# Performance work log

Hardware: AMD Instinct MI355X
Metric: run time of the kernel (lower is better)

Reference implementation:

```python
import jax, jax.numpy as jnp
import numpy as np

N = 50000      # nodes
E = 800000     # edges (avg degree 16)
IN = 64        # in_channels
H = 128        # hidden_channels
OUT = 64       # out_channels
G = 64         # number of graphs in batch


def setup_inputs() -> dict:
    key = jax.random.key(0)
    ks = jax.random.split(key, 16)
    x = jax.random.normal(ks[0], (N, IN), dtype=jnp.float32)
    edge_index = jax.random.randint(ks[1], (2, E), 0, N, dtype=jnp.int64)
    batch = jnp.sort(jax.random.randint(ks[2], (N,), 0, G, dtype=jnp.int64))
    s = 0.05
    return {
        "x": x,
        "edge_index": edge_index,
        "batch": batch,
        # SAGEConv1: out = aggr @ W_l + x @ W_r + b
        "W1l": jax.random.normal(ks[3], (IN, H), dtype=jnp.float32) * s,
        "W1r": jax.random.normal(ks[4], (IN, H), dtype=jnp.float32) * s,
        "b1": jnp.zeros((H,), dtype=jnp.float32),
        # SAGEConv2
        "W2l": jax.random.normal(ks[5], (H, H), dtype=jnp.float32) * s,
        "W2r": jax.random.normal(ks[6], (H, H), dtype=jnp.float32) * s,
        "b2": jnp.zeros((H,), dtype=jnp.float32),
        # MLP head
        "W3": jax.random.normal(ks[7], (H, H), dtype=jnp.float32) * s,
        "b3": jnp.zeros((H,), dtype=jnp.float32),
        "W4": jax.random.normal(ks[8], (H, OUT), dtype=jnp.float32) * s,
        "b4": jnp.zeros((OUT,), dtype=jnp.float32),
    }


def sage_conv(x, src, dst, Wl, Wr, b, n_nodes):
    # mean-aggregate neighbor (source) features onto target nodes
    msgs = x[src]                                            # [E, d] gather
    agg = jax.ops.segment_sum(msgs, dst, num_segments=n_nodes)
    cnt = jax.ops.segment_sum(jnp.ones((src.shape[0],), x.dtype), dst,
                              num_segments=n_nodes)
    agg = agg / jnp.maximum(cnt, 1.0)[:, None]               # mean, 0 if no nbrs
    return agg @ Wl + x @ Wr + b


def reference(x, edge_index, batch, W1l, W1r, b1, W2l, W2r, b2, W3, b3, W4, b4):
    src, dst = edge_index[0], edge_index[1]
    n = x.shape[0]
    h = jax.nn.elu(sage_conv(x, src, dst, W1l, W1r, b1, n))   # dropout: eval mode (no-op)
    h = jax.nn.elu(sage_conv(h, src, dst, W2l, W2r, b2, n))
    # global mean pool per graph
    gsum = jax.ops.segment_sum(h, batch, num_segments=G)
    gcnt = jax.ops.segment_sum(jnp.ones((n,), h.dtype), batch, num_segments=G)
    gmean = gsum / jnp.maximum(gcnt, 1.0)[:, None]
    # global max pool per graph
    gmax = jax.ops.segment_max(h, batch, num_segments=G)
    pool = gmean + gmax                                       # [G, H]
    out = jax.nn.relu(pool @ W3 + b3) @ W4 + b4               # [G, OUT]
    return out
```

## Files before the change

### kernel.cpp

```cpp
#include <hip/hip_runtime.h>
#include <math.h>

constexpr int HDIM = 128;
constexpr int GRAPHS = 64;
constexpr int OUTD = 64;
constexpr int BK_SHIFT = 7;
constexpr int BK_NODES = 1 << BK_SHIFT;
constexpr int BK_CAP   = 2560;

typedef __attribute__((ext_vector_type(8))) short bf16x8;
typedef __attribute__((ext_vector_type(8))) unsigned short us8;
typedef __attribute__((ext_vector_type(4))) unsigned short us4;
typedef __attribute__((ext_vector_type(4))) float f32x4;

__device__ inline float bf2f(unsigned short u) {
  return __uint_as_float(((unsigned int)u) << 16);
}
__device__ inline unsigned short f2bf(float x) {
  unsigned int u = __float_as_uint(x);
  return (unsigned short)((u + 0x7FFF + ((u >> 16) & 1)) >> 16);
}

__device__ inline void atomicMaxF(float* addr, float v) {
  if (v >= 0.0f) atomicMax((int*)addr, __float_as_int(v));
  else           atomicMin((unsigned int*)addr, __float_as_uint(v));
}

__device__ inline void pack_body(const float* __restrict__ W, unsigned short* __restrict__ P,
                                 int K, int tid) {
  int lane = tid & 63, frag = tid >> 6;
  int t = frag >> 3, ct = frag & 7;
  int kb = t * 32 + (lane >> 4) * 8;
  int col = ct * 16 + (lane & 15);
  us8 o;
#pragma unroll
  for (int i = 0; i < 8; i++) o[i] = f2bf(W[(size_t)(kb + i) * HDIM + col]);
  *(us8*)(P + (size_t)tid * 8) = o;
}

__global__ __launch_bounds__(256) void prep_k(
    const float* __restrict__ x, unsigned short* __restrict__ x_b, int nx4,
    const float* __restrict__ W1l, const float* __restrict__ W1r,
    const float* __restrict__ W2l, const float* __restrict__ W2r,
    unsigned short* w1l_p, unsigned short* w1r_p,
    unsigned short* w2l_p, unsigned short* w2r_p,
    int* __restrict__ gcnt, int nbk,
    float* __restrict__ gsum, float* __restrict__ gmax,
    const int* __restrict__ batch, int* __restrict__ gstart, int n) {
  const int b = blockIdx.x, t = threadIdx.x;
  if (b < 4)        pack_body(W1l, w1l_p, 64,  b * 256 + t);
  else if (b < 8)   pack_body(W1r, w1r_p, 64,  (b - 4) * 256 + t);
  else if (b < 16)  pack_body(W2l, w2l_p, 128, (b - 8) * 256 + t);
  else if (b < 24)  pack_body(W2r, w2r_p, 128, (b - 16) * 256 + t);
  else if (b == 24) { for (int i = t; i < nbk; i += 256) gcnt[i] = 0; }
  else if (b == 25) {
    for (int i = t; i < GRAPHS * HDIM; i += 256) { gsum[i] = 0.0f; gmax[i] = -INFINITY; }
  } else if (b == 26) {
    if (t <= GRAPHS) {
      int g = t;
      int lo = 0, hi = n;
      while (lo < hi) {
        int mid = (lo + hi) >> 1;
        if (batch[mid] < g) lo = mid + 1; else hi = mid;
      }
      gstart[g] = (g == GRAPHS) ? n : lo;
    }
  } else {
    for (int i = (b - 27) * 256 + t; i < nx4; i += 256 * 256) {
      float4 v = ((const float4*)x)[i];
      us4 o = { f2bf(v.x), f2bf(v.y), f2bf(v.z), f2bf(v.w) };
      *((us4*)x_b + i) = o;
    }
  }
}

__global__ __launch_bounds__(256) void partition_k(const int* __restrict__ src,
                                                   const int* __restrict__ dst,
                                                   int* __restrict__ gcnt,
                                                   int* __restrict__ ebuf,
                                                   int E, int nbk) {
  __shared__ int hist[512];
  __shared__ int lcur[512];
  __shared__ int rbase[512];
  const int t = threadIdx.x;
  int tile = (E + gridDim.x - 1) / gridDim.x;
  int e0 = blockIdx.x * tile;
  int e1 = min(E, e0 + tile);
  for (int i = t; i < 512; i += 256) { hist[i] = 0; lcur[i] = 0; }
  __syncthreads();
  for (int e = e0 + t; e < e1; e += 256)
    atomicAdd(&hist[dst[e] >> BK_SHIFT], 1);
  __syncthreads();
  for (int b = t; b < nbk; b += 256)
    if (hist[b] > 0) rbase[b] = atomicAdd(&gcnt[b], hist[b]);
  __syncthreads();
  for (int e = e0 + t; e < e1; e += 256) {
    int d = dst[e];
    int b = d >> BK_SHIFT;
    int slot = rbase[b] + atomicAdd(&lcur[b], 1);
    if (slot < BK_CAP)
      ebuf[(size_t)b * BK_CAP + slot] = ((d & (BK_NODES - 1)) << 20) | src[e];
  }
}

__global__ __launch_bounds__(256) void perm_build_k(const int* __restrict__ ebuf,
                                                    const int* __restrict__ gcnt,
                                                    int* __restrict__ offs,
                                                    int* __restrict__ perm, int n) {
  __shared__ int st[BK_CAP];
  __shared__ int perm_st[BK_CAP];
  __shared__ int nh[BK_NODES];
  __shared__ int excl_s[BK_NODES];
  __shared__ int lc[BK_NODES];
  __shared__ int psum[256];
  const int b = blockIdx.x;
  const int t = threadIdx.x;
  const int nodeBase = b << BK_SHIFT;
  const int cnt = min(gcnt[b], BK_CAP);

  int part = 0;
  for (int i = t; i < b; i += 256) part += gcnt[i];
  psum[t] = part;
  for (int i = t; i < BK_NODES; i += 256) nh[i] = 0;
  __syncthreads();
#pragma unroll
  for (int s2 = 128; s2 > 0; s2 >>= 1) {
    if (t < s2) psum[t] += psum[t + s2];
    __syncthreads();
  }
  const int bb = psum[0];

  for (int i = t; i < cnt; i += 256) {
    int e = ebuf[(size_t)b * BK_CAP + i];
    st[i] = e;
    atomicAdd(&nh[e >> 20], 1);
  }
  __syncthreads();
  if (t < 64) {
    int v0 = nh[t];
    int incl = v0;
#pragma unroll
    for (int d = 1; d < 64; d <<= 1) {
      int u = __shfl_up(incl, d, 64);
      if (t >= d) incl += u;
    }
    excl_s[t] = incl - v0;
    int tot0 = __shfl(incl, 63, 64);
    int v1 = nh[64 + t];
    int incl1 = v1;
#pragma unroll
    for (int d = 1; d < 64; d <<= 1) {
      int u = __shfl_up(incl1, d, 64);
      if (t >= d) incl1 += u;
    }
    excl_s[64 + t] = tot0 + incl1 - v1;
  }
  __syncthreads();
  for (int i = t; i < BK_NODES; i += 256) {
    int idx = nodeBase + i;
    if (idx <= n) offs[idx] = bb + excl_s[i];
  }
  for (int i = t; i < BK_NODES; i += 256) lc[i] = excl_s[i];
  __syncthreads();
  for (int i = t; i < cnt; i += 256) {
    int e = st[i];
    int slot = atomicAdd(&lc[e >> 20], 1);
    perm_st[slot] = e & 0xFFFFF;
  }
  __syncthreads();
  for (int i = t; i < cnt; i += 256) perm[bb + i] = perm_st[i];
}

template<int K, int ROWS, bool POOL>
__global__ __launch_bounds__(256) void sage_fused_k(
    const unsigned short* __restrict__ feat,
    const int* __restrict__ offs, const int* __restrict__ perm,
    const unsigned short* __restrict__ B0, const unsigned short* __restrict__ B1,
    const float* __restrict__ bias, unsigned short* __restrict__ out,
    const int* __restrict__ batch, float* __restrict__ gsum, float* __restrict__ gmax,
    int n) {
  constexpr int NT = K / 32;
  constexpr int C8 = K / 8;
  constexpr int SR = K + 24;
  constexpr int RPP = 256 / C8;
  constexpr int PASSES = (ROWS + RPP - 1) / RPP;
  constexpr int RT = ROWS / 16;
  constexpr int WPR = 4 / RT;
  constexpr int CTW = 8 / WPR;
  constexpr int PSR = HDIM + 8;
  __shared__ unsigned short a_lds[ROWS * SR];
  __shared__ int batch_s[ROWS];
  const int t = threadIdx.x;
  const int rowBase = blockIdx.x * ROWS;

#pragma unroll
  for (int p = 0; p < PASSES; p++) {
    int lr = p * RPP + t / C8;
    int c8 = t % C8;
    int row = rowBase + lr;
    if (lr < ROWS && row < n) {
      int s = offs[row], e = offs[row + 1];
      float acc[8] = {0.f, 0.f, 0.f, 0.f, 0.f, 0.f, 0.f, 0.f};
      const unsigned short* fb = feat + c8 * 8;
      int j = s;
      for (; j + 3 < e; j += 4) {
        int r0 = perm[j], r1 = perm[j + 1], r2 = perm[j + 2], r3 = perm[j + 3];
        us8 v0 = *(const us8*)(fb + (size_t)r0 * K);
        us8 v1 = *(const us8*)(fb + (size_t)r1 * K);
        us8 v2 = *(const us8*)(fb + (size_t)r2 * K);
        us8 v3 = *(const us8*)(fb + (size_t)r3 * K);
#pragma unroll
        for (int q = 0; q < 8; q++)
          acc[q] += (bf2f(v0[q]) + bf2f(v1[q])) + (bf2f(v2[q]) + bf2f(v3[q]));
      }
      for (; j < e; j++) {
        int r = perm[j];
        us8 v = *(const us8*)(fb + (size_t)r * K);
#pragma unroll
        for (int q = 0; q < 8; q++) acc[q] += bf2f(v[q]);
      }
      float sc = 1.0f / fmaxf((float)(e - s), 1.0f);
      us8 o;
#pragma unroll
      for (int q = 0; q < 8; q++) o[q] = f2bf(acc[q] * sc);
      *(us8*)(a_lds + lr * SR + c8 * 8) = o;
    }
  }
  if (POOL && t < ROWS) {
    int row = rowBase + t;
    batch_s[t] = (row < n) ? batch[row] : -1;
  }
  __syncthreads();

  const int lane = t & 63;
  const int w = t >> 6;
  const int rh = w / WPR;
  const int cw = w % WPR;
  const int row0 = rowBase + rh * 16;
  const int l16 = lane & 15, lhi = lane >> 4;
  f32x4 acc[CTW];
#pragma unroll
  for (int cc = 0; cc < CTW; cc++) acc[cc] = (f32x4){0.f, 0.f, 0.f, 0.f};
  const unsigned short* al = a_lds + (rh * 16 + l16) * SR + lhi * 8;
  const unsigned short* ag = feat + (size_t)min(row0 + l16, n - 1) * K + lhi * 8;
#pragma unroll
  for (int t2 = 0; t2 < NT; t2++) {
    bf16x8 afA = *(const bf16x8*)(al + t2 * 32);
    bf16x8 afS = *(const bf16x8*)(ag + t2 * 32);
#pragma unroll
    for (int cc = 0; cc < CTW; cc++) {
      int ct = cw * CTW + cc;
      bf16x8 b0 = *(const bf16x8*)(B0 + ((size_t)(t2 * 8 + ct) * 64 + lane) * 8);
      acc[cc] = __builtin_amdgcn_mfma_f32_16x16x32_bf16(afA, b0, acc[cc], 0, 0, 0);
      bf16x8 b1 = *(const bf16x8*)(B1 + ((size_t)(t2 * 8 + ct) * 64 + lane) * 8);
      acc[cc] = __builtin_amdgcn_mfma_f32_16x16x32_bf16(afS, b1, acc[cc], 0, 0, 0);
    }
  }

  if constexpr (!POOL) {
#pragma unroll
    for (int cc = 0; cc < CTW; cc++) {
      int col = (cw * CTW + cc) * 16 + l16;
      float bs = bias[col];
#pragma unroll
      for (int i = 0; i < 4; i++) {
        int row = row0 + lhi * 4 + i;
        if (row < n) {
          float v = acc[cc][i] + bs;
          v = (v > 0.f) ? v : expm1f(v);
          out[(size_t)row * HDIM + col] = f2bf(v);
        }
      }
    }
  } else {
    __syncthreads();
    unsigned short* ptile = a_lds;
#pragma unroll
    for (int cc = 0; cc < CTW; cc++) {
      int col = (cw * CTW + cc) * 16 + l16;
      float bs = bias[col];
#pragma unroll
      for (int i = 0; i < 4; i++) {
        int rl = rh * 16 + lhi * 4 + i;
        float v = acc[cc][i] + bs;
        v = (v > 0.f) ? v : expm1f(v);
        ptile[rl * PSR + col] = f2bf(v);
      }
    }
    __syncthreads();
    int c = t & 127;
    int half = t >> 7;
    float sum = 0.0f, mx = -INFINITY;
    int gc = -1;
    for (int r = half * (ROWS / 2); r < (half + 1) * (ROWS / 2); r++) {
      int g = batch_s[r];
      if (g < 0) continue;
      float v = bf2f(ptile[r * PSR + c]);
      if (g != gc) {
        if (gc >= 0) {
          atomicAdd(&gsum[gc * HDIM + c], sum);
          atomicMaxF(&gmax[gc * HDIM + c], mx);
        }
        gc = g; sum = 0.0f; mx = -INFINITY;
      }
      sum += v;
      mx = fmaxf(mx, v);
    }
    if (gc >= 0) {
      atomicAdd(&gsum[gc * HDIM + c], sum);
      atomicMaxF(&gmax[gc * HDIM + c], mx);
    }
  }
}

__global__ __launch_bounds__(128) void head_k(
    const float* __restrict__ gsum, const float* __restrict__ gmax,
    const int* __restrict__ gstart,
    const float* __restrict__ W3, const float* __restrict__ b3,
    const float* __restrict__ W4, const float* __restrict__ b4,
    float* __restrict__ out) {
  __shared__ float pool_s[HDIM];
  __shared__ float t1_s[HDIM];
  int g = blockIdx.x, c = threadIdx.x;
  float cntf = (float)(gstart[g + 1] - gstart[g]);
  float ic = 1.0f / fmaxf(cntf, 1.0f);
  pool_s[c] = gsum[g * HDIM + c] * ic + gmax[g * HDIM + c];
  __syncthreads();
  float acc = b3[c];
  for (int k = 0; k < HDIM; k++) acc += pool_s[k] * W3[k * HDIM + c];
  t1_s[c] = fmaxf(acc, 0.0f);
  __syncthreads();
  if (c < OUTD) {
    float acc2 = b4[c];
    for (int k = 0; k < HDIM; k++) acc2 += t1_s[k] * W4[k * OUTD + c];
    out[g * OUTD + c] = acc2;
  }
}

extern "C" void kernel_launch(void* const* d_in, const int* in_sizes, int n_in,
                              void* d_out, int out_size, void* d_ws, size_t ws_size,
                              hipStream_t stream) {
  const float* x     = (const float*)d_in[0];
  const int*   ei    = (const int*)d_in[1];
  const int*   batch = (const int*)d_in[2];
  const float* W1l = (const float*)d_in[3];
  const float* W1r = (const float*)d_in[4];
  const float* b1  = (const float*)d_in[5];
  const float* W2l = (const float*)d_in[6];
  const float* W2r = (const float*)d_in[7];
  const float* b2  = (const float*)d_in[8];
  const float* W3  = (const float*)d_in[9];
  const float* b3  = (const float*)d_in[10];
  const float* W4  = (const float*)d_in[11];
  const float* b4  = (const float*)d_in[12];

  const int N  = in_sizes[2];
  const int E  = in_sizes[1] / 2;
  const int IN = in_sizes[0] / N;
  const int* src = ei;
  const int* dst = ei + E;
  const int NBK = (N + BK_NODES - 1) / BK_NODES;

  char* ws = (char*)d_ws;
  size_t off = 0;
  auto alloc = [&](size_t bytes) { void* p = ws + off; off += (bytes + 255) & ~(size_t)255; return p; };
  int*  offs  = (int*)alloc((size_t)(N + 1) * 4);
  int*  perm  = (int*)alloc((size_t)E * 4);
  int*  gcnt  = (int*)alloc((size_t)NBK * 4);
  int*  ebuf  = (int*)alloc((size_t)NBK * BK_CAP * 4);
  unsigned short* x_b   = (unsigned short*)alloc((size_t)N * IN * 2);
  unsigned short* h1_b  = (unsigned short*)alloc((size_t)N * HDIM * 2);
  unsigned short* w1l_p = (unsigned short*)alloc((size_t)IN * HDIM * 2);
  unsigned short* w1r_p = (unsigned short*)alloc((size_t)IN * HDIM * 2);
  unsigned short* w2l_p = (unsigned short*)alloc((size_t)HDIM * HDIM * 2);
  unsigned short* w2r_p = (unsigned short*)alloc((size_t)HDIM * HDIM * 2);
  float* gsum = (float*)alloc((size_t)GRAPHS * HDIM * 4);
  float* gmax = (float*)alloc((size_t)GRAPHS * HDIM * 4);
  int* gstart = (int*)alloc((size_t)(GRAPHS + 1) * 4);
  (void)ws_size; (void)n_in; (void)out_size;

  prep_k<<<283, 256, 0, stream>>>(x, x_b, N * IN / 4, W1l, W1r, W2l, W2r,
                                  w1l_p, w1r_p, w2l_p, w2r_p, gcnt, NBK, gsum, gmax,
                                  batch, gstart, N);

  partition_k<<<256, 256, 0, stream>>>(src, dst, gcnt, ebuf, E, NBK);
  perm_build_k<<<NBK, 256, 0, stream>>>(ebuf, gcnt, offs, perm, N);

  sage_fused_k<64, 32, false><<<(N + 31) / 32, 256, 0, stream>>>(
      x_b, offs, perm, w1l_p, w1r_p, b1, h1_b, nullptr, nullptr, nullptr, N);

  sage_fused_k<128, 32, true><<<(N + 31) / 32, 256, 0, stream>>>(
      h1_b, offs, perm, w2l_p, w2r_p, b2, nullptr, batch, gsum, gmax, N);

  head_k<<<GRAPHS, 128, 0, stream>>>(gsum, gmax, gstart, W3, b3, W4, b4, (float*)d_out);
}
```

Before: 107.5 us.

## Merge prep, partition and perm-build into one cooperative kernel with grid sync

```diff
diff --git a/kernel.cpp b/kernel.cpp
--- a/kernel.cpp
+++ b/kernel.cpp
@@ -1,5 +1,8 @@
 #include <hip/hip_runtime.h>
+#include <hip/hip_cooperative_groups.h>
 #include <math.h>
+
+namespace cg = cooperative_groups;
 
 constexpr int HDIM = 128;
 constexpr int GRAPHS = 64;
@@ -7,6 +10,7 @@
 constexpr int BK_SHIFT = 7;
 constexpr int BK_NODES = 1 << BK_SHIFT;
 constexpr int BK_CAP   = 2560;
+constexpr int PART_BLKS = 256;
 
 typedef __attribute__((ext_vector_type(8))) short bf16x8;
 typedef __attribute__((ext_vector_type(8))) unsigned short us8;
@@ -38,24 +42,55 @@
   *(us8*)(P + (size_t)tid * 8) = o;
 }
 
-__global__ __launch_bounds__(256) void prep_k(
+__global__ __launch_bounds__(256) void build_k(
+    const int* __restrict__ src, const int* __restrict__ dst,
+    int* __restrict__ gcnt, int* __restrict__ ebuf, int E, int nbk,
     const float* __restrict__ x, unsigned short* __restrict__ x_b, int nx4,
     const float* __restrict__ W1l, const float* __restrict__ W1r,
     const float* __restrict__ W2l, const float* __restrict__ W2r,
     unsigned short* w1l_p, unsigned short* w1r_p,
     unsigned short* w2l_p, unsigned short* w2r_p,
-    int* __restrict__ gcnt, int nbk,
     float* __restrict__ gsum, float* __restrict__ gmax,
-    const int* __restrict__ batch, int* __restrict__ gstart, int n) {
-  const int b = blockIdx.x, t = threadIdx.x;
-  if (b < 4)        pack_body(W1l, w1l_p, 64,  b * 256 + t);
-  else if (b < 8)   pack_body(W1r, w1r_p, 64,  (b - 4) * 256 + t);
-  else if (b < 16)  pack_body(W2l, w2l_p, 128, (b - 8) * 256 + t);
-  else if (b < 24)  pack_body(W2r, w2r_p, 128, (b - 16) * 256 + t);
-  else if (b == 24) { for (int i = t; i < nbk; i += 256) gcnt[i] = 0; }
-  else if (b == 25) {
+    const int* __restrict__ batch, int* __restrict__ gstart, int n,
+    int* __restrict__ offs, int* __restrict__ perm) {
+  __shared__ int hist[512];
+  __shared__ int lcur[512];
+  __shared__ int rbase[512];
+  __shared__ int st[BK_CAP];
+  __shared__ int perm_st[BK_CAP];
+  __shared__ int nh[BK_NODES];
+  __shared__ int excl_s[BK_NODES];
+  __shared__ int lc[BK_NODES];
+  __shared__ int psum[256];
+  const int t = threadIdx.x;
+  const int b = blockIdx.x;
+
+  if (b < PART_BLKS) {
+    int tile = (E + PART_BLKS - 1) / PART_BLKS;
+    int e0 = b * tile;
+    int e1 = min(E, e0 + tile);
+    for (int i = t; i < 512; i += 256) { hist[i] = 0; lcur[i] = 0; }
+    __syncthreads();
+    for (int e = e0 + t; e < e1; e += 256)
+      atomicAdd(&hist[dst[e] >> BK_SHIFT], 1);
+    __syncthreads();
+    for (int bk = t; bk < nbk; bk += 256)
+      if (hist[bk] > 0) rbase[bk] = atomicAdd(&gcnt[bk], hist[bk]);
+    __syncthreads();
+    for (int e = e0 + t; e < e1; e += 256) {
+      int d = dst[e];
+      int bk = d >> BK_SHIFT;
+      int slot = rbase[bk] + atomicAdd(&lcur[bk], 1);
+      if (slot < BK_CAP)
+        ebuf[(size_t)bk * BK_CAP + slot] = ((d & (BK_NODES - 1)) << 20) | src[e];
+    }
+  } else if (b < PART_BLKS + 4)       pack_body(W1l, w1l_p, 64,  (b - PART_BLKS) * 256 + t);
+  else if (b < PART_BLKS + 8)         pack_body(W1r, w1r_p, 64,  (b - PART_BLKS - 4) * 256 + t);
+  else if (b < PART_BLKS + 16)        pack_body(W2l, w2l_p, 128, (b - PART_BLKS - 8) * 256 + t);
+  else if (b < PART_BLKS + 24)        pack_body(W2r, w2r_p, 128, (b - PART_BLKS - 16) * 256 + t);
+  else if (b == PART_BLKS + 24) {
     for (int i = t; i < GRAPHS * HDIM; i += 256) { gsum[i] = 0.0f; gmax[i] = -INFINITY; }
-  } else if (b == 26) {
+  } else if (b == PART_BLKS + 25) {
     if (t <= GRAPHS) {
       int g = t;
       int lo = 0, hi = n;
@@ -66,55 +101,17 @@
       gstart[g] = (g == GRAPHS) ? n : lo;
     }
   } else {
-    for (int i = (b - 27) * 256 + t; i < nx4; i += 256 * 256) {
+    const int cb = b - (PART_BLKS + 26);
+    const int ncb = gridDim.x - (PART_BLKS + 26);
+    for (int i = cb * 256 + t; i < nx4; i += ncb * 256) {
       float4 v = ((const float4*)x)[i];
       us4 o = { f2bf(v.x), f2bf(v.y), f2bf(v.z), f2bf(v.w) };
       *((us4*)x_b + i) = o;
     }
   }
-}
-
-__global__ __launch_bounds__(256) void partition_k(const int* __restrict__ src,
-                                                   const int* __restrict__ dst,
-                                                   int* __restrict__ gcnt,
-                                                   int* __restrict__ ebuf,
-                                                   int E, int nbk) {
-  __shared__ int hist[512];
-  __shared__ int lcur[512];
-  __shared__ int rbase[512];
-  const int t = threadIdx.x;
-  int tile = (E + gridDim.x - 1) / gridDim.x;
-  int e0 = blockIdx.x * tile;
-  int e1 = min(E, e0 + tile);
-  for (int i = t; i < 512; i += 256) { hist[i] = 0; lcur[i] = 0; }
-  __syncthreads();
-  for (int e = e0 + t; e < e1; e += 256)
-    atomicAdd(&hist[dst[e] >> BK_SHIFT], 1);
-  __syncthreads();
-  for (int b = t; b < nbk; b += 256)
-    if (hist[b] > 0) rbase[b] = atomicAdd(&gcnt[b], hist[b]);
-  __syncthreads();
-  for (int e = e0 + t; e < e1; e += 256) {
-    int d = dst[e];
-    int b = d >> BK_SHIFT;
-    int slot = rbase[b] + atomicAdd(&lcur[b], 1);
-    if (slot < BK_CAP)
-      ebuf[(size_t)b * BK_CAP + slot] = ((d & (BK_NODES - 1)) << 20) | src[e];
-  }
-}
-
-__global__ __launch_bounds__(256) void perm_build_k(const int* __restrict__ ebuf,
-                                                    const int* __restrict__ gcnt,
-                                                    int* __restrict__ offs,
-                                                    int* __restrict__ perm, int n) {
-  __shared__ int st[BK_CAP];
-  __shared__ int perm_st[BK_CAP];
-  __shared__ int nh[BK_NODES];
-  __shared__ int excl_s[BK_NODES];
-  __shared__ int lc[BK_NODES];
-  __shared__ int psum[256];
-  const int b = blockIdx.x;
-  const int t = threadIdx.x;
+
+  cg::this_grid().sync();
+
   const int nodeBase = b << BK_SHIFT;
   const int cnt = min(gcnt[b], BK_CAP);
 
@@ -379,12 +376,17 @@
   int* gstart = (int*)alloc((size_t)(GRAPHS + 1) * 4);
   (void)ws_size; (void)n_in; (void)out_size;
 
-  prep_k<<<283, 256, 0, stream>>>(x, x_b, N * IN / 4, W1l, W1r, W2l, W2r,
-                                  w1l_p, w1r_p, w2l_p, w2r_p, gcnt, NBK, gsum, gmax,
-                                  batch, gstart, N);
-
-  partition_k<<<256, 256, 0, stream>>>(src, dst, gcnt, ebuf, E, NBK);
-  perm_build_k<<<NBK, 256, 0, stream>>>(ebuf, gcnt, offs, perm, N);
+  hipMemsetAsync(gcnt, 0, (size_t)NBK * 4, stream);
+  int nx4 = N * IN / 4;
+  void* kargs[] = {
+    (void*)&src, (void*)&dst, (void*)&gcnt, (void*)&ebuf, (void*)&E, (void*)&NBK,
+    (void*)&x, (void*)&x_b, (void*)&nx4,
+    (void*)&W1l, (void*)&W1r, (void*)&W2l, (void*)&W2r,
+    (void*)&w1l_p, (void*)&w1r_p, (void*)&w2l_p, (void*)&w2r_p,
+    (void*)&gsum, (void*)&gmax, (void*)&batch, (void*)&gstart, (void*)&N,
+    (void*)&offs, (void*)&perm
+  };
+  hipLaunchCooperativeKernel((void*)build_k, dim3(NBK), dim3(256), kargs, 0, stream);
 
   sage_fused_k<64, 32, false><<<(N + 31) / 32, 256, 0, stream>>>(
       x_b, offs, perm, w1l_p, w1r_p, b1, h1_b, nullptr, nullptr, nullptr, N);
```

Result: slower. 183.0 us (+70.2%).
